# Optimization experiments

Measured on AMD Instinct MI355X. Metric: run time of the kernel, lower is better.

## Reference

```python
import jax, jax.numpy as jnp
import numpy as np

S, N, M = 8, 4096, 64          # snapshots, atoms, total neighbors (sum of max_num_neighs)
L = 20.0                        # periodic box length
R_CS, R_C = 2.0, 6.0            # smooth cutoff radii
DSUB = 16                       # dim_sub_net
PAD_FRAC = 0.15                 # fraction of -1 padded neighbor slots


def _mlp(x, params):
    # DenseChainNet: Linear -> relu between layers, no activation after last layer
    n = len(params)
    for i, (W, b) in enumerate(params):
        x = x @ W + b
        if i < n - 1:
            x = jax.nn.relu(x)
    return x


def _lin(k, fan_in, fan_out):
    k1, k2 = jax.random.split(k)
    s = 1.0 / np.sqrt(fan_in)
    W = jax.random.uniform(k1, (fan_in, fan_out), minval=-s, maxval=s, dtype=jnp.float32)
    b = jax.random.uniform(k2, (fan_out,), minval=-s, maxval=s, dtype=jnp.float32)
    return W, b


def setup_inputs() -> dict:
    key = jax.random.key(0)
    ks = jax.random.split(key, 12)
    inputs = jax.random.uniform(ks[0], (S, N, 3), dtype=jnp.float32) * L
    input_types = jax.random.randint(ks[1], (S, N), 0, 2)
    # neighbor indices, guaranteed != self, with -1 padding
    base = jnp.arange(N, dtype=jnp.int32)[None, :, None]
    off = jax.random.randint(ks[2], (S, N, M), 1, N)
    neigh = (base + off) % N
    pad = jax.random.uniform(ks[3], (S, N, M)) < PAD_FRAC
    neigh_list = jnp.where(pad, -1, neigh).astype(jnp.int32)
    es1_w, es1_b = _lin(ks[4], 2, 4)
    es2_w, es2_b = _lin(ks[5], 4, 4)
    fs1_w, fs1_b = _lin(ks[6], 4, 4)
    fs2_w, fs2_b = _lin(ks[7], 4, 4)
    en1_w, en1_b = _lin(ks[8], 4, 8)
    en2_w, en2_b = _lin(ks[9], 8, 16)
    en3_w, en3_b = _lin(ks[10], 16, 32)
    return dict(inputs=inputs, input_types=input_types, neigh_list=neigh_list,
                es1_w=es1_w, es1_b=es1_b, es2_w=es2_w, es2_b=es2_b,
                fs1_w=fs1_w, fs1_b=fs1_b, fs2_w=fs2_w, fs2_b=fs2_b,
                en1_w=en1_w, en1_b=en1_b, en2_w=en2_w, en2_b=en2_b,
                en3_w=en3_w, en3_b=en3_b)


def reference(inputs, input_types, neigh_list,
              es1_w, es1_b, es2_w, es2_b,
              fs1_w, fs1_b, fs2_w, fs2_b,
              en1_w, en1_b, en2_w, en2_b, en3_w, en3_b):
    mask = neigh_list == -1                               # [S,N,M]
    idx = jnp.where(mask, 0, neigh_list)
    flat = idx.reshape(S, N * M)
    # gather neighbor coordinates with periodic minimum-image convention
    pos_j = jnp.take_along_axis(inputs, flat[..., None], axis=1).reshape(S, N, M, 3)
    d = pos_j - inputs[:, :, None, :]
    d = d - L * jnp.round(d / L)
    r = jnp.sqrt(jnp.sum(d * d, axis=-1) + 1e-12)         # [S,N,M]
    # smooth cutoff: s(r) = 1/r for r<r_cs, cosine switch to 0 at r_c
    u = (r - R_CS) / (R_C - R_CS)
    sw = jnp.where(r < R_CS, 1.0,
                   jnp.where(r < R_C, 0.5 * jnp.cos(jnp.pi * u) + 0.5, 0.0))
    s_ij = jnp.where(mask, 0.0, sw / r)                   # [S,N,M]
    r_ij = d * (s_ij / r)[..., None]                      # s(r) * d / r, [S,N,M,3]
    # species pair descriptor (symmetrized over pair order)
    neigh_types = jnp.take_along_axis(input_types, flat, axis=1).reshape(S, N, M)
    self_t = jnp.broadcast_to(input_types[:, :, None], (S, N, M))
    pairs = jnp.stack([self_t, neigh_types], axis=-1).astype(jnp.float32).reshape(-1, 2)
    es = [(es1_w, es1_b), (es2_w, es2_b)]
    td = _mlp(pairs, es) + _mlp(pairs[:, ::-1], es)
    td = _mlp(td, [(fs1_w, fs1_b), (fs2_w, fs2_b)]).reshape(S, N, M, -1)  # [S,N,M,4]
    s_tilde = (td * s_ij[..., None]).reshape(S * N * M, -1)
    G = _mlp(s_tilde, [(en1_w, en1_b), (en2_w, en2_b), (en3_w, en3_b)]).reshape(S, N, M, -1)  # [S,N,M,32]
    r_tilde = jnp.concatenate([s_ij[..., None], r_ij], axis=-1)            # [S,N,M,4]
    R = jnp.einsum('snmd,snmk->sndk', r_tilde, G[..., :DSUB])              # [S,N,4,16]
    R1 = jnp.einsum('snmd,sndk->snmk', r_tilde, R)                         # [S,N,M,16]
    D = jnp.einsum('snmg,snmk->sngk', G, R1)                               # [S,N,32,16]
    return D
```

## Files before the change

kernel.cpp:

```cpp
#include <hip/hip_runtime.h>
#include <math.h>

#define SS 8
#define NN 4096
#define MM 64
#define LBOX 20.0f

typedef __attribute__((ext_vector_type(8)))  short    short8;
typedef __attribute__((ext_vector_type(2)))  float    floatx2;
typedef __attribute__((ext_vector_type(4)))  float    floatx4;
typedef __attribute__((ext_vector_type(2)))  __bf16   bf16x2;

__device__ inline unsigned pkbf(float a, float b) {
    bf16x2 p; p.x = (__bf16)a; p.y = (__bf16)b;
    unsigned u; __builtin_memcpy(&u, &p, 4); return u;
}

__global__ __launch_bounds__(256) void desc_kernel(
    const float* __restrict__ pos,
    const int*   __restrict__ types,
    const int*   __restrict__ neigh,
    const float* __restrict__ es1_w, const float* __restrict__ es1_b,
    const float* __restrict__ es2_w, const float* __restrict__ es2_b,
    const float* __restrict__ fs1_w, const float* __restrict__ fs1_b,
    const float* __restrict__ fs2_w, const float* __restrict__ fs2_b,
    const float* __restrict__ en1_w, const float* __restrict__ en1_b,
    const float* __restrict__ en2_w, const float* __restrict__ en2_b,
    const float* __restrict__ en3_w, const float* __restrict__ en3_b,
    float* __restrict__ out)
{
    __shared__ alignas(16) unsigned short sh_h2[4][16][72];
    __shared__ alignas(16) unsigned short sh_rt[4][4][72];
    __shared__ alignas(16) float sh_PT[4][4][20];
    __shared__ alignas(16) float sh_W3p[512];
    __shared__ alignas(16) float sh_b3p[16][2];
    __shared__ alignas(16) float sh_A[4][128];
    __shared__ alignas(16) float sh_vt[4][8];

    const int tid = threadIdx.x;

    if (tid < 4) {
        const float ti = (float)(tid >> 1), tj = (float)(tid & 1);
        float e[4] = {0.f, 0.f, 0.f, 0.f};
        #pragma unroll
        for (int swp = 0; swp < 2; ++swp) {
            const float a = swp ? tj : ti, b = swp ? ti : tj;
            float h[4];
            #pragma unroll
            for (int k = 0; k < 4; ++k)
                h[k] = fmaxf(a * es1_w[k] + b * es1_w[4 + k] + es1_b[k], 0.f);
            #pragma unroll
            for (int k = 0; k < 4; ++k) {
                float acc = es2_b[k];
                #pragma unroll
                for (int j = 0; j < 4; ++j) acc += h[j] * es2_w[j * 4 + k];
                e[k] += acc;
            }
        }
        float f[4];
        #pragma unroll
        for (int k = 0; k < 4; ++k) {
            float acc = fs1_b[k];
            #pragma unroll
            for (int j = 0; j < 4; ++j) acc += e[j] * fs1_w[j * 4 + k];
            f[k] = fmaxf(acc, 0.f);
        }
        float td[4];
        #pragma unroll
        for (int k = 0; k < 4; ++k) {
            float acc = fs2_b[k];
            #pragma unroll
            for (int j = 0; j < 4; ++j) acc += f[j] * fs2_w[j * 4 + k];
            td[k] = acc;
        }
        #pragma unroll
        for (int o = 0; o < 8; ++o) {
            float acc = 0.f;
            #pragma unroll
            for (int d = 0; d < 4; ++d) acc += td[d] * en1_w[d * 8 + o];
            sh_vt[tid][o] = acc;
        }
    }
    #pragma unroll
    for (int rr = 0; rr < 2; ++rr) {
        const int i = tid + rr * 256;
        const int hp = i >> 6, g = (i >> 2) & 15, w = i & 3;
        sh_W3p[i] = en3_w[(2 * hp + (w >> 1)) * 32 + g + 16 * (w & 1)];
    }
    if (tid < 32) sh_b3p[tid >> 1][tid & 1] = en3_b[(tid & 1) * 16 + (tid >> 1)];
    __syncthreads();

    const int wave = tid >> 6;
    const int lane = tid & 63;
    const int atomBase = blockIdx.x * 16 + wave * 4;
    const int sbase = atomBase & ~(NN - 1);

    int   nb_c = neigh[atomBase * MM + lane];
    int   gj_c = sbase + (nb_c < 0 ? 0 : nb_c);
    float px_c = pos[gj_c * 3 + 0];
    float py_c = pos[gj_c * 3 + 1];
    float pz_c = pos[gj_c * 3 + 2];
    int   tj_c = types[gj_c];

    #pragma unroll
    for (int a = 0; a < 4; ++a) {
        const int atom = atomBase + a;
        const int   nb  = nb_c;
        const float pxx = px_c, pyy = py_c, pzz = pz_c;
        const int   tjv = tj_c;

        int nb_n = 0;
        if (a < 3) nb_n = neigh[(atom + 1) * MM + lane];

        const float xi = pos[atom * 3 + 0];
        const float yi = pos[atom * 3 + 1];
        const float zi = pos[atom * 3 + 2];
        const int   ti = types[atom];

        const int msk = nb < 0;
        float dx = pxx - xi;
        float dy = pyy - yi;
        float dz = pzz - zi;
        dx -= LBOX * rintf(dx * (1.0f / LBOX));
        dy -= LBOX * rintf(dy * (1.0f / LBOX));
        dz -= LBOX * rintf(dz * (1.0f / LBOX));
        const float r2   = fmaf(dx, dx, fmaf(dy, dy, fmaf(dz, dz, 1e-12f)));
        const float rinv = rsqrtf(r2);
        const float r    = r2 * rinv;
        const float u    = fminf(fmaxf((r - 2.0f) * 0.25f, 0.0f), 1.0f);
        const float swv  = 0.5f * __cosf(3.14159265358979323846f * u) + 0.5f;
        const float sij   = msk ? 0.0f : swv * rinv;
        const float scale = sij * rinv;
        const int   tt    = ti * 2 + tjv;

        float h1[8];
        {
            const float4 va = *(const float4*)(&sh_vt[tt][0]);
            const float4 vb = *(const float4*)(&sh_vt[tt][4]);
            h1[0] = fmaxf(fmaf(sij, va.x, en1_b[0]), 0.f);
            h1[1] = fmaxf(fmaf(sij, va.y, en1_b[1]), 0.f);
            h1[2] = fmaxf(fmaf(sij, va.z, en1_b[2]), 0.f);
            h1[3] = fmaxf(fmaf(sij, va.w, en1_b[3]), 0.f);
            h1[4] = fmaxf(fmaf(sij, vb.x, en1_b[4]), 0.f);
            h1[5] = fmaxf(fmaf(sij, vb.y, en1_b[5]), 0.f);
            h1[6] = fmaxf(fmaf(sij, vb.z, en1_b[6]), 0.f);
            h1[7] = fmaxf(fmaf(sij, vb.w, en1_b[7]), 0.f);
        }

        #pragma unroll
        for (int k = 0; k < 16; ++k) {
            float acc = en2_b[k];
            #pragma unroll
            for (int i = 0; i < 8; ++i) acc = fmaf(h1[i], en2_w[i * 16 + k], acc);
            const unsigned pk = pkbf(fmaxf(acc, 0.f), 0.f);
            sh_h2[wave][k][lane] = (unsigned short)pk;
        }
        {
            const unsigned p0 = pkbf(sij, dx * scale), p1 = pkbf(dy * scale, dz * scale);
            sh_rt[wave][0][lane] = (unsigned short)p0;
            sh_rt[wave][1][lane] = (unsigned short)(p0 >> 16);
            sh_rt[wave][2][lane] = (unsigned short)p1;
            sh_rt[wave][3][lane] = (unsigned short)(p1 >> 16);
        }

        if (a < 3) {
            gj_c = sbase + (nb_n < 0 ? 0 : nb_n);
            px_c = pos[gj_c * 3 + 0];
            py_c = pos[gj_c * 3 + 1];
            pz_c = pos[gj_c * 3 + 2];
            tj_c = types[gj_c];
            nb_c = nb_n;
        }

        asm volatile("s_waitcnt lgkmcnt(0)" ::: "memory");

        const int col16 = lane & 15;
        const int q4    = lane >> 4;
        const int m0    = q4 * 8;
        floatx4 cP = {0.f, 0.f, 0.f, 0.f};
        floatx4 cQ = {0.f, 0.f, 0.f, 0.f};
        const short8 ones = (short8)(short)0x3F80;
        #pragma unroll
        for (int ck = 0; ck < 2; ++ck) {
            const short8 af = *(const short8*)&sh_h2[wave][col16][ck * 32 + m0];
            const short8 bf = *(const short8*)&sh_rt[wave][col16 & 3][ck * 32 + m0];
            cP = __builtin_amdgcn_mfma_f32_16x16x32_bf16(af, bf, cP, 0, 0, 0);
            cQ = __builtin_amdgcn_mfma_f32_16x16x32_bf16(ones, bf, cQ, 0, 0, 0);
        }
        if (col16 < 4) *(floatx4*)&sh_PT[wave][col16][q4 * 4] = cP;
        const float qd = cQ[0];
        asm volatile("s_waitcnt lgkmcnt(0)" ::: "memory");

        {
            const int g0 = lane >> 2, dd = lane & 3;
            const floatx2 b3v = *(const floatx2*)&sh_b3p[g0][0];
            floatx2 acc2 = floatx2{qd, qd} * b3v;
            #pragma unroll
            for (int h4 = 0; h4 < 4; ++h4) {
                const floatx4 pv = *(const floatx4*)&sh_PT[wave][dd][h4 * 4];
                const floatx4 wa = *(const floatx4*)&sh_W3p[(h4 * 2 + 0) * 64 + g0 * 4];
                const floatx4 wb = *(const floatx4*)&sh_W3p[(h4 * 2 + 1) * 64 + g0 * 4];
                acc2 += floatx2{pv.x, pv.x} * floatx2{wa.x, wa.y};
                acc2 += floatx2{pv.y, pv.y} * floatx2{wa.z, wa.w};
                acc2 += floatx2{pv.z, pv.z} * floatx2{wb.x, wb.y};
                acc2 += floatx2{pv.w, pv.w} * floatx2{wb.z, wb.w};
            }
            sh_A[wave][lane]      = acc2.x;
            sh_A[wave][lane + 64] = acc2.y;
        }
        asm volatile("s_waitcnt lgkmcnt(0)" ::: "memory");

        {
            const int g = lane >> 1, koff = (lane & 1) * 8;
            const floatx4 Ag = *(const floatx4*)&sh_A[wave][g * 4];
            floatx4 o0, o1;
            #pragma unroll
            for (int jj = 0; jj < 8; ++jj) {
                const floatx4 Ak = *(const floatx4*)&sh_A[wave][(koff + jj) * 4];
                const float v = fmaf(Ag.x, Ak.x, fmaf(Ag.y, Ak.y, fmaf(Ag.z, Ak.z, Ag.w * Ak.w)));
                if (jj < 4) o0[jj] = v; else o1[jj - 4] = v;
            }
            float* op = out + (size_t)atom * 512 + lane * 8;
            __builtin_nontemporal_store(o0, (floatx4*)op);
            __builtin_nontemporal_store(o1, (floatx4*)(op + 4));
        }
        asm volatile("s_waitcnt lgkmcnt(0)" ::: "memory");
    }
}

extern "C" void kernel_launch(void* const* d_in, const int* in_sizes, int n_in,
                              void* d_out, int out_size, void* d_ws, size_t ws_size,
                              hipStream_t stream) {
    const float* pos   = (const float*)d_in[0];
    const int*   typ   = (const int*)d_in[1];
    const int*   ngh   = (const int*)d_in[2];
    desc_kernel<<<dim3((SS * NN) / 16), dim3(256), 0, stream>>>(
        pos, typ, ngh,
        (const float*)d_in[3],  (const float*)d_in[4],
        (const float*)d_in[5],  (const float*)d_in[6],
        (const float*)d_in[7],  (const float*)d_in[8],
        (const float*)d_in[9],  (const float*)d_in[10],
        (const float*)d_in[11], (const float*)d_in[12],
        (const float*)d_in[13], (const float*)d_in[14],
        (const float*)d_in[15], (const float*)d_in[16],
        (float*)d_out);
}
```

Measured before the change: 133.6 us.

## Add prep kernel packing positions/types and precomputing weight tables; one atom per wave

A new prep kernel packs positions and types into float4 records in the workspace and precomputes the species-pair table and the permuted en3 weights once, instead of every block recomputing them. The main kernel then does one 16-byte gather per neighbour and handles one atom per wave across four times as many blocks, dropping the four-atom software-pipelined loop. This trades an extra launch plus a workspace round trip for less redundant per-block setup and more parallelism. It also loses the prefetch overlap between consecutive atoms.

```diff
diff --git a/kernel.cpp b/kernel.cpp
--- a/kernel.cpp
+++ b/kernel.cpp
@@ -16,17 +16,91 @@
     unsigned u; __builtin_memcpy(&u, &p, 4); return u;
 }
 
-__global__ __launch_bounds__(256) void desc_kernel(
-    const float* __restrict__ pos,
-    const int*   __restrict__ types,
-    const int*   __restrict__ neigh,
+#define WS_POSW   0
+#define WS_WT     (524288 / 4)
+#define WT_VT     0
+#define WT_B3P    32
+#define WT_W3P    64
+
+__global__ __launch_bounds__(256) void prep_kernel(
+    const float* __restrict__ pos, const int* __restrict__ types,
     const float* __restrict__ es1_w, const float* __restrict__ es1_b,
     const float* __restrict__ es2_w, const float* __restrict__ es2_b,
     const float* __restrict__ fs1_w, const float* __restrict__ fs1_b,
     const float* __restrict__ fs2_w, const float* __restrict__ fs2_b,
-    const float* __restrict__ en1_w, const float* __restrict__ en1_b,
+    const float* __restrict__ en1_w, const float* __restrict__ en3_w,
+    const float* __restrict__ en3_b, float* __restrict__ ws)
+{
+    const int tid = threadIdx.x;
+    const int b = blockIdx.x;
+    if (b < 128) {
+        const int i = b * 256 + tid;
+        floatx4 v;
+        v.x = pos[i * 3 + 0];
+        v.y = pos[i * 3 + 1];
+        v.z = pos[i * 3 + 2];
+        v.w = __int_as_float(types[i]);
+        *((floatx4*)ws + i) = v;
+        return;
+    }
+    float* wt = ws + WS_WT;
+    if (tid < 4) {
+        const float ti = (float)(tid >> 1), tj = (float)(tid & 1);
+        float e[4] = {0.f, 0.f, 0.f, 0.f};
+        #pragma unroll
+        for (int swp = 0; swp < 2; ++swp) {
+            const float a = swp ? tj : ti, bb = swp ? ti : tj;
+            float h[4];
+            #pragma unroll
+            for (int k = 0; k < 4; ++k)
+                h[k] = fmaxf(a * es1_w[k] + bb * es1_w[4 + k] + es1_b[k], 0.f);
+            #pragma unroll
+            for (int k = 0; k < 4; ++k) {
+                float acc = es2_b[k];
+                #pragma unroll
+                for (int j = 0; j < 4; ++j) acc += h[j] * es2_w[j * 4 + k];
+                e[k] += acc;
+            }
+        }
+        float f[4];
+        #pragma unroll
+        for (int k = 0; k < 4; ++k) {
+            float acc = fs1_b[k];
+            #pragma unroll
+            for (int j = 0; j < 4; ++j) acc += e[j] * fs1_w[j * 4 + k];
+            f[k] = fmaxf(acc, 0.f);
+        }
+        float td[4];
+        #pragma unroll
+        for (int k = 0; k < 4; ++k) {
+            float acc = fs2_b[k];
+            #pragma unroll
+            for (int j = 0; j < 4; ++j) acc += f[j] * fs2_w[j * 4 + k];
+            td[k] = acc;
+        }
+        #pragma unroll
+        for (int o = 0; o < 8; ++o) {
+            float acc = 0.f;
+            #pragma unroll
+            for (int d = 0; d < 4; ++d) acc += td[d] * en1_w[d * 8 + o];
+            wt[WT_VT + tid * 8 + o] = acc;
+        }
+    }
+    if (tid < 32)
+        wt[WT_B3P + tid] = en3_b[(tid & 1) * 16 + (tid >> 1)];
+    #pragma unroll
+    for (int rr = 0; rr < 2; ++rr) {
+        const int i = tid + rr * 256;
+        const int hp = i >> 6, g = (i >> 2) & 15, w = i & 3;
+        wt[WT_W3P + i] = en3_w[(2 * hp + (w >> 1)) * 32 + g + 16 * (w & 1)];
+    }
+}
+
+__global__ __launch_bounds__(256) void desc_kernel(
+    const float* __restrict__ ws,
+    const int*   __restrict__ neigh,
+    const float* __restrict__ en1_b,
     const float* __restrict__ en2_w, const float* __restrict__ en2_b,
-    const float* __restrict__ en3_w, const float* __restrict__ en3_b,
     float* __restrict__ out)
 {
     __shared__ alignas(16) unsigned short sh_h2[4][16][72];
@@ -38,193 +112,126 @@
     __shared__ alignas(16) float sh_vt[4][8];
 
     const int tid = threadIdx.x;
-
-    if (tid < 4) {
-        const float ti = (float)(tid >> 1), tj = (float)(tid & 1);
-        float e[4] = {0.f, 0.f, 0.f, 0.f};
-        #pragma unroll
-        for (int swp = 0; swp < 2; ++swp) {
-            const float a = swp ? tj : ti, b = swp ? ti : tj;
-            float h[4];
-            #pragma unroll
-            for (int k = 0; k < 4; ++k)
-                h[k] = fmaxf(a * es1_w[k] + b * es1_w[4 + k] + es1_b[k], 0.f);
-            #pragma unroll
-            for (int k = 0; k < 4; ++k) {
-                float acc = es2_b[k];
-                #pragma unroll
-                for (int j = 0; j < 4; ++j) acc += h[j] * es2_w[j * 4 + k];
-                e[k] += acc;
-            }
-        }
-        float f[4];
-        #pragma unroll
-        for (int k = 0; k < 4; ++k) {
-            float acc = fs1_b[k];
-            #pragma unroll
-            for (int j = 0; j < 4; ++j) acc += e[j] * fs1_w[j * 4 + k];
-            f[k] = fmaxf(acc, 0.f);
-        }
-        float td[4];
-        #pragma unroll
-        for (int k = 0; k < 4; ++k) {
-            float acc = fs2_b[k];
-            #pragma unroll
-            for (int j = 0; j < 4; ++j) acc += f[j] * fs2_w[j * 4 + k];
-            td[k] = acc;
-        }
-        #pragma unroll
-        for (int o = 0; o < 8; ++o) {
-            float acc = 0.f;
-            #pragma unroll
-            for (int d = 0; d < 4; ++d) acc += td[d] * en1_w[d * 8 + o];
-            sh_vt[tid][o] = acc;
-        }
-    }
+    const float* wt = ws + WS_WT;
+
+    if (tid < 32) {
+        ((float*)sh_vt)[tid]  = wt[WT_VT + tid];
+        ((float*)sh_b3p)[tid] = wt[WT_B3P + tid];
+    }
+    sh_W3p[tid]       = wt[WT_W3P + tid];
+    sh_W3p[tid + 256] = wt[WT_W3P + 256 + tid];
+    __syncthreads();
+
+    const int wave = __builtin_amdgcn_readfirstlane(tid >> 6);
+    const int lane = tid & 63;
+    const int atom = __builtin_amdgcn_readfirstlane(blockIdx.x * 4 + (tid >> 6));
+    const int sbase = atom & ~(NN - 1);
+    const floatx4* __restrict__ pw = (const floatx4*)ws;
+
+    const floatx4 pi4 = pw[atom];
+    const float xi = pi4.x, yi = pi4.y, zi = pi4.z;
+    const int   ti = __float_as_int(pi4.w);
+
+    const int nb  = neigh[atom * MM + lane];
+    const int msk = nb < 0;
+    const int gj  = sbase + (msk ? 0 : nb);
+    const floatx4 pj4 = pw[gj];
+    const int tj = __float_as_int(pj4.w);
+
+    float dx = pj4.x - xi;
+    float dy = pj4.y - yi;
+    float dz = pj4.z - zi;
+    dx -= LBOX * rintf(dx * (1.0f / LBOX));
+    dy -= LBOX * rintf(dy * (1.0f / LBOX));
+    dz -= LBOX * rintf(dz * (1.0f / LBOX));
+    const float r2   = fmaf(dx, dx, fmaf(dy, dy, fmaf(dz, dz, 1e-12f)));
+    const float rinv = rsqrtf(r2);
+    const float r    = r2 * rinv;
+    const float u    = fminf(fmaxf((r - 2.0f) * 0.25f, 0.0f), 1.0f);
+    const float swv  = 0.5f * __cosf(3.14159265358979323846f * u) + 0.5f;
+    const float sij   = msk ? 0.0f : swv * rinv;
+    const float scale = sij * rinv;
+    const int   tt    = ti * 2 + tj;
+
+    float h1[8];
+    {
+        const float4 va = *(const float4*)(&sh_vt[tt][0]);
+        const float4 vb = *(const float4*)(&sh_vt[tt][4]);
+        h1[0] = fmaxf(fmaf(sij, va.x, en1_b[0]), 0.f);
+        h1[1] = fmaxf(fmaf(sij, va.y, en1_b[1]), 0.f);
+        h1[2] = fmaxf(fmaf(sij, va.z, en1_b[2]), 0.f);
+        h1[3] = fmaxf(fmaf(sij, va.w, en1_b[3]), 0.f);
+        h1[4] = fmaxf(fmaf(sij, vb.x, en1_b[4]), 0.f);
+        h1[5] = fmaxf(fmaf(sij, vb.y, en1_b[5]), 0.f);
+        h1[6] = fmaxf(fmaf(sij, vb.z, en1_b[6]), 0.f);
+        h1[7] = fmaxf(fmaf(sij, vb.w, en1_b[7]), 0.f);
+    }
+
     #pragma unroll
-    for (int rr = 0; rr < 2; ++rr) {
-        const int i = tid + rr * 256;
-        const int hp = i >> 6, g = (i >> 2) & 15, w = i & 3;
-        sh_W3p[i] = en3_w[(2 * hp + (w >> 1)) * 32 + g + 16 * (w & 1)];
-    }
-    if (tid < 32) sh_b3p[tid >> 1][tid & 1] = en3_b[(tid & 1) * 16 + (tid >> 1)];
-    __syncthreads();
-
-    const int wave = tid >> 6;
-    const int lane = tid & 63;
-    const int atomBase = blockIdx.x * 16 + wave * 4;
-    const int sbase = atomBase & ~(NN - 1);
-
-    int   nb_c = neigh[atomBase * MM + lane];
-    int   gj_c = sbase + (nb_c < 0 ? 0 : nb_c);
-    float px_c = pos[gj_c * 3 + 0];
-    float py_c = pos[gj_c * 3 + 1];
-    float pz_c = pos[gj_c * 3 + 2];
-    int   tj_c = types[gj_c];
-
+    for (int k = 0; k < 16; ++k) {
+        float acc = en2_b[k];
+        #pragma unroll
+        for (int i = 0; i < 8; ++i) acc = fmaf(h1[i], en2_w[i * 16 + k], acc);
+        sh_h2[wave][k][lane] = (unsigned short)pkbf(fmaxf(acc, 0.f), 0.f);
+    }
+    {
+        const unsigned p0 = pkbf(sij, dx * scale), p1 = pkbf(dy * scale, dz * scale);
+        sh_rt[wave][0][lane] = (unsigned short)p0;
+        sh_rt[wave][1][lane] = (unsigned short)(p0 >> 16);
+        sh_rt[wave][2][lane] = (unsigned short)p1;
+        sh_rt[wave][3][lane] = (unsigned short)(p1 >> 16);
+    }
+    asm volatile("s_waitcnt lgkmcnt(0)" ::: "memory");
+
+    const int col16 = lane & 15;
+    const int q4    = lane >> 4;
+    const int m0    = q4 * 8;
+    floatx4 cP = {0.f, 0.f, 0.f, 0.f};
+    floatx4 cQ = {0.f, 0.f, 0.f, 0.f};
+    const short8 ones = (short8)(short)0x3F80;
     #pragma unroll
-    for (int a = 0; a < 4; ++a) {
-        const int atom = atomBase + a;
-        const int   nb  = nb_c;
-        const float pxx = px_c, pyy = py_c, pzz = pz_c;
-        const int   tjv = tj_c;
-
-        int nb_n = 0;
-        if (a < 3) nb_n = neigh[(atom + 1) * MM + lane];
-
-        const float xi = pos[atom * 3 + 0];
-        const float yi = pos[atom * 3 + 1];
-        const float zi = pos[atom * 3 + 2];
-        const int   ti = types[atom];
-
-        const int msk = nb < 0;
-        float dx = pxx - xi;
-        float dy = pyy - yi;
-        float dz = pzz - zi;
-        dx -= LBOX * rintf(dx * (1.0f / LBOX));
-        dy -= LBOX * rintf(dy * (1.0f / LBOX));
-        dz -= LBOX * rintf(dz * (1.0f / LBOX));
-        const float r2   = fmaf(dx, dx, fmaf(dy, dy, fmaf(dz, dz, 1e-12f)));
-        const float rinv = rsqrtf(r2);
-        const float r    = r2 * rinv;
-        const float u    = fminf(fmaxf((r - 2.0f) * 0.25f, 0.0f), 1.0f);
-        const float swv  = 0.5f * __cosf(3.14159265358979323846f * u) + 0.5f;
-        const float sij   = msk ? 0.0f : swv * rinv;
-        const float scale = sij * rinv;
-        const int   tt    = ti * 2 + tjv;
-
-        float h1[8];
-        {
-            const float4 va = *(const float4*)(&sh_vt[tt][0]);
-            const float4 vb = *(const float4*)(&sh_vt[tt][4]);
-            h1[0] = fmaxf(fmaf(sij, va.x, en1_b[0]), 0.f);
-            h1[1] = fmaxf(fmaf(sij, va.y, en1_b[1]), 0.f);
-            h1[2] = fmaxf(fmaf(sij, va.z, en1_b[2]), 0.f);
-            h1[3] = fmaxf(fmaf(sij, va.w, en1_b[3]), 0.f);
-            h1[4] = fmaxf(fmaf(sij, vb.x, en1_b[4]), 0.f);
-            h1[5] = fmaxf(fmaf(sij, vb.y, en1_b[5]), 0.f);
-            h1[6] = fmaxf(fmaf(sij, vb.z, en1_b[6]), 0.f);
-            h1[7] = fmaxf(fmaf(sij, vb.w, en1_b[7]), 0.f);
-        }
-
-        #pragma unroll
-        for (int k = 0; k < 16; ++k) {
-            float acc = en2_b[k];
-            #pragma unroll
-            for (int i = 0; i < 8; ++i) acc = fmaf(h1[i], en2_w[i * 16 + k], acc);
-            const unsigned pk = pkbf(fmaxf(acc, 0.f), 0.f);
-            sh_h2[wave][k][lane] = (unsigned short)pk;
-        }
-        {
-            const unsigned p0 = pkbf(sij, dx * scale), p1 = pkbf(dy * scale, dz * scale);
-            sh_rt[wave][0][lane] = (unsigned short)p0;
-            sh_rt[wave][1][lane] = (unsigned short)(p0 >> 16);
-            sh_rt[wave][2][lane] = (unsigned short)p1;
-            sh_rt[wave][3][lane] = (unsigned short)(p1 >> 16);
-        }
-
-        if (a < 3) {
-            gj_c = sbase + (nb_n < 0 ? 0 : nb_n);
-            px_c = pos[gj_c * 3 + 0];
-            py_c = pos[gj_c * 3 + 1];
-            pz_c = pos[gj_c * 3 + 2];
-            tj_c = types[gj_c];
-            nb_c = nb_n;
-        }
-
-        asm volatile("s_waitcnt lgkmcnt(0)" ::: "memory");
-
-        const int col16 = lane & 15;
-        const int q4    = lane >> 4;
-        const int m0    = q4 * 8;
-        floatx4 cP = {0.f, 0.f, 0.f, 0.f};
-        floatx4 cQ = {0.f, 0.f, 0.f, 0.f};
-        const short8 ones = (short8)(short)0x3F80;
-        #pragma unroll
-        for (int ck = 0; ck < 2; ++ck) {
-            const short8 af = *(const short8*)&sh_h2[wave][col16][ck * 32 + m0];
-            const short8 bf = *(const short8*)&sh_rt[wave][col16 & 3][ck * 32 + m0];
-            cP = __builtin_amdgcn_mfma_f32_16x16x32_bf16(af, bf, cP, 0, 0, 0);
-            cQ = __builtin_amdgcn_mfma_f32_16x16x32_bf16(ones, bf, cQ, 0, 0, 0);
-        }
-        if (col16 < 4) *(floatx4*)&sh_PT[wave][col16][q4 * 4] = cP;
-        const float qd = cQ[0];
-        asm volatile("s_waitcnt lgkmcnt(0)" ::: "memory");
-
-        {
-            const int g0 = lane >> 2, dd = lane & 3;
-            const floatx2 b3v = *(const floatx2*)&sh_b3p[g0][0];
-            floatx2 acc2 = floatx2{qd, qd} * b3v;
-            #pragma unroll
-            for (int h4 = 0; h4 < 4; ++h4) {
-                const floatx4 pv = *(const floatx4*)&sh_PT[wave][dd][h4 * 4];
-                const floatx4 wa = *(const floatx4*)&sh_W3p[(h4 * 2 + 0) * 64 + g0 * 4];
-                const floatx4 wb = *(const floatx4*)&sh_W3p[(h4 * 2 + 1) * 64 + g0 * 4];
-                acc2 += floatx2{pv.x, pv.x} * floatx2{wa.x, wa.y};
-                acc2 += floatx2{pv.y, pv.y} * floatx2{wa.z, wa.w};
-                acc2 += floatx2{pv.z, pv.z} * floatx2{wb.x, wb.y};
-                acc2 += floatx2{pv.w, pv.w} * floatx2{wb.z, wb.w};
-            }
-            sh_A[wave][lane]      = acc2.x;
-            sh_A[wave][lane + 64] = acc2.y;
-        }
-        asm volatile("s_waitcnt lgkmcnt(0)" ::: "memory");
-
-        {
-            const int g = lane >> 1, koff = (lane & 1) * 8;
-            const floatx4 Ag = *(const floatx4*)&sh_A[wave][g * 4];
-            floatx4 o0, o1;
-            #pragma unroll
-            for (int jj = 0; jj < 8; ++jj) {
-                const floatx4 Ak = *(const floatx4*)&sh_A[wave][(koff + jj) * 4];
-                const float v = fmaf(Ag.x, Ak.x, fmaf(Ag.y, Ak.y, fmaf(Ag.z, Ak.z, Ag.w * Ak.w)));
-                if (jj < 4) o0[jj] = v; else o1[jj - 4] = v;
-            }
-            float* op = out + (size_t)atom * 512 + lane * 8;
-            __builtin_nontemporal_store(o0, (floatx4*)op);
-            __builtin_nontemporal_store(o1, (floatx4*)(op + 4));
-        }
-        asm volatile("s_waitcnt lgkmcnt(0)" ::: "memory");
+    for (int ck = 0; ck < 2; ++ck) {
+        const short8 af = *(const short8*)&sh_h2[wave][col16][ck * 32 + m0];
+        const short8 bf = *(const short8*)&sh_rt[wave][col16 & 3][ck * 32 + m0];
+        cP = __builtin_amdgcn_mfma_f32_16x16x32_bf16(af, bf, cP, 0, 0, 0);
+        cQ = __builtin_amdgcn_mfma_f32_16x16x32_bf16(ones, bf, cQ, 0, 0, 0);
+    }
+    if (col16 < 4) *(floatx4*)&sh_PT[wave][col16][q4 * 4] = cP;
+    const float qd = cQ[0];
+    asm volatile("s_waitcnt lgkmcnt(0)" ::: "memory");
+
+    {
+        const int g0 = lane >> 2, dd = lane & 3;
+        const floatx2 b3v = *(const floatx2*)&sh_b3p[g0][0];
+        floatx2 acc2 = floatx2{qd, qd} * b3v;
+        #pragma unroll
+        for (int h4 = 0; h4 < 4; ++h4) {
+            const floatx4 pv = *(const floatx4*)&sh_PT[wave][dd][h4 * 4];
+            const floatx4 wa = *(const floatx4*)&sh_W3p[(h4 * 2 + 0) * 64 + g0 * 4];
+            const floatx4 wb = *(const floatx4*)&sh_W3p[(h4 * 2 + 1) * 64 + g0 * 4];
+            acc2 += floatx2{pv.x, pv.x} * floatx2{wa.x, wa.y};
+            acc2 += floatx2{pv.y, pv.y} * floatx2{wa.z, wa.w};
+            acc2 += floatx2{pv.z, pv.z} * floatx2{wb.x, wb.y};
+            acc2 += floatx2{pv.w, pv.w} * floatx2{wb.z, wb.w};
+        }
+        sh_A[wave][lane]      = acc2.x;
+        sh_A[wave][lane + 64] = acc2.y;
+    }
+    asm volatile("s_waitcnt lgkmcnt(0)" ::: "memory");
+
+    {
+        const int g = lane >> 1, koff = (lane & 1) * 8;
+        const floatx4 Ag = *(const floatx4*)&sh_A[wave][g * 4];
+        floatx4 o0, o1;
+        #pragma unroll
+        for (int jj = 0; jj < 8; ++jj) {
+            const floatx4 Ak = *(const floatx4*)&sh_A[wave][(koff + jj) * 4];
+            const float v = fmaf(Ag.x, Ak.x, fmaf(Ag.y, Ak.y, fmaf(Ag.z, Ak.z, Ag.w * Ak.w)));
+            if (jj < 4) o0[jj] = v; else o1[jj - 4] = v;
+        }
+        float* op = out + (size_t)atom * 512 + lane * 8;
+        __builtin_nontemporal_store(o0, (floatx4*)op);
+        __builtin_nontemporal_store(o1, (floatx4*)(op + 4));
     }
 }
 
@@ -234,14 +241,21 @@
     const float* pos   = (const float*)d_in[0];
     const int*   typ   = (const int*)d_in[1];
     const int*   ngh   = (const int*)d_in[2];
-    desc_kernel<<<dim3((SS * NN) / 16), dim3(256), 0, stream>>>(
-        pos, typ, ngh,
+    float* ws = (float*)d_ws;
+
+    prep_kernel<<<dim3(129), dim3(256), 0, stream>>>(
+        pos, typ,
         (const float*)d_in[3],  (const float*)d_in[4],
         (const float*)d_in[5],  (const float*)d_in[6],
         (const float*)d_in[7],  (const float*)d_in[8],
         (const float*)d_in[9],  (const float*)d_in[10],
-        (const float*)d_in[11], (const float*)d_in[12],
+        (const float*)d_in[11],
+        (const float*)d_in[15], (const float*)d_in[16],
+        ws);
+
+    desc_kernel<<<dim3((SS * NN) / 4), dim3(256), 0, stream>>>(
+        ws, ngh,
+        (const float*)d_in[12],
         (const float*)d_in[13], (const float*)d_in[14],
-        (const float*)d_in[15], (const float*)d_in[16],
         (float*)d_out);
 }
```

Result: faster. 125.1 us (-6.3%).
